# Performance work log

Hardware: AMD Instinct MI355X
Metric: run time of the kernel (lower is better)

Reference implementation:

```python
import jax, jax.numpy as jnp
import numpy as np

B, NUM, NVAR = 2048, 100, 11
NUM_OBS, NC = 10, 3
T_FIN = 10.0
RHO_OBS = 1.0; RHO_INEQ = 1.0; RHO_LANE = 1.0; RHO_PROJ = 1.0
W_SMOOTH = 20.0; W_VDES = 2.0; W_YDES = 1.0
A_EGO = 3.0; B_EGO = 1.5; MARGIN = 0.2
V_MIN = 0.001; V_MAX = 18.0; A_MAX = 6.0
MAXITER = 5
H = 256

def _basis():
    s = np.linspace(0.0, 1.0, NUM)
    j = np.arange(NVAR)
    P = s[:, None] ** j[None, :]
    Pd = np.zeros((NUM, NVAR)); Pdd = np.zeros((NUM, NVAR))
    Pd[:, 1:] = j[1:][None, :] * s[:, None] ** (j[1:] - 1)[None, :]
    Pdd[:, 2:] = (j[2:] * (j[2:] - 1))[None, :] * s[:, None] ** (j[2:] - 2)[None, :]
    return (jnp.asarray(P, jnp.float32), jnp.asarray(Pd / T_FIN, jnp.float32),
            jnp.asarray(Pdd / (T_FIN ** 2), jnp.float32))

P, PDOT, PDDOT = _basis()
A_EQ_X = jnp.stack([P[0], PDOT[0], PDDOT[0], P[-1]])   # [4, NVAR]
A_EQ_Y = jnp.stack([P[0], PDOT[0], PDDOT[0]])          # [3, NVAR]
PTP = P.T @ P

def _kkt_inv(Q, A):
    m = A.shape[0]
    K = jnp.concatenate([jnp.concatenate([Q, A.T], axis=1),
                         jnp.concatenate([A, jnp.zeros((m, m), jnp.float32)], axis=1)], axis=0)
    return jnp.linalg.inv(K)

# ADMM cost: rho_proj*I + smoothness + rho_obs*A_obs^T A_obs + rho_ineq*(Pdot^T Pdot + Pddot^T Pddot)
Q_COMMON = (RHO_PROJ + W_SMOOTH) * jnp.eye(NVAR, dtype=jnp.float32) \
    + RHO_OBS * NUM_OBS * NC * PTP \
    + RHO_INEQ * (PDOT.T @ PDOT + PDDOT.T @ PDDOT)
KKT_X = _kkt_inv(Q_COMMON, A_EQ_X)
KKT_Y = _kkt_inv(Q_COMMON + 2.0 * RHO_LANE * PTP, A_EQ_Y)   # A_lane = [P; -P]
# x_init QP (smoothness + v_des / y_des tracking)
Q_IX = W_SMOOTH * jnp.eye(NVAR, dtype=jnp.float32) + W_VDES * (PDOT.T @ PDOT)
KKT_IX = _kkt_inv(Q_IX, A_EQ_X)
KKT_IY = _kkt_inv(Q_IX + W_YDES * PTP, A_EQ_Y)


def _forward(init_state_ego, goal_des, closest_obs, psi_obs, dim_x_obs, dim_y_obs,
             y_ub, y_lb, gru_W_ih, gru_W_hh, gru_b, gru_h0,
             mlp_W1, mlp_b1, mlp_W2, mlp_b2):
    b = init_state_ego.shape[0]
    x0, y0, vx0, vy0, ax0, ay0 = (init_state_ego[:, i] for i in range(6))
    b_eq_x = jnp.stack([x0, vx0, ax0, goal_des[:, 0]], axis=1)   # [B,4]
    b_eq_y = jnp.stack([y0, vy0, ay0], axis=1)                    # [B,3]

    # ---- obstacle circle trajectories (static obstacles, vx=vy=0) ----
    xo = closest_obs[:, :NUM_OBS]; yo = closest_obs[:, NUM_OBS:2 * NUM_OBS]   # [B,O]
    r = jnp.stack([jnp.zeros_like(dim_x_obs),
                   (dim_x_obs - dim_y_obs) / 2,
                   -(dim_x_obs - dim_y_obs) / 2], axis=2)                      # [B,O,3]
    x_circ = xo[:, :, None] + r * jnp.cos(psi_obs)[:, :, None]                # [B,O,3]
    y_circ = yo[:, :, None] + r * jnp.sin(psi_obs)[:, :, None]
    shape4 = (b, NUM_OBS, NC, NUM)
    x_obs_f = jnp.broadcast_to(x_circ[..., None], shape4).reshape(b, -1)      # [B,O*C*T]
    y_obs_f = jnp.broadcast_to(y_circ[..., None], shape4).reshape(b, -1)
    rad = dim_y_obs / 2
    a_obs = jnp.broadcast_to((A_EGO + rad + MARGIN)[:, :, None, None], shape4).reshape(b, -1)
    b_obs = jnp.broadcast_to((B_EGO + rad + MARGIN)[:, :, None, None], shape4).reshape(b, -1)

    # ---- GRU context over obstacles -> learned lambda init ----
    feats = jnp.stack([xo, yo, dim_x_obs, dim_y_obs, psi_obs], axis=2)        # [B,O,5]
    def gru_step(h, x):
        gx = x @ gru_W_ih + gru_b
        gh = h @ gru_W_hh
        z = jax.nn.sigmoid(gx[:, :H] + gh[:, :H])
        rg = jax.nn.sigmoid(gx[:, H:2 * H] + gh[:, H:2 * H])
        n = jnp.tanh(gx[:, 2 * H:] + rg * gh[:, 2 * H:])
        return (1.0 - z) * n + z * h, None
    hT, _ = jax.lax.scan(gru_step, jnp.broadcast_to(gru_h0, (b, H)), jnp.swapaxes(feats, 0, 1))
    lam = jax.nn.relu(hT @ mlp_W1 + mlp_b1) @ mlp_W2 + mlp_b2                 # [B,2*NVAR]
    lam_x, lam_y = lam[:, :NVAR], lam[:, NVAR:]

    # ---- x_init: equality-constrained smoothness/tracking QP ----
    v_des = jnp.sqrt(vx0 ** 2 + vy0 ** 2)
    lin_ix = W_VDES * v_des[:, None] * jnp.sum(PDOT, axis=0)[None, :]
    lin_iy = W_YDES * goal_des[:, 1:2] * jnp.sum(P, axis=0)[None, :]
    c_x0 = (jnp.concatenate([lin_ix, b_eq_x], 1) @ KKT_IX.T)[:, :NVAR]
    c_y0 = (jnp.concatenate([lin_iy, b_eq_y], 1) @ KKT_IY.T)[:, :NVAR]

    b_lane = jnp.concatenate([y_ub[:, None] * jnp.ones((1, NUM), jnp.float32),
                              -y_lb[:, None] * jnp.ones((1, NUM), jnp.float32)], axis=1)  # [B,2T]

    def AobsT(v):   # A_obs^T v, v: [B, O*C*T] -> [B, NVAR]
        return v.reshape(b, NUM_OBS * NC, NUM).sum(axis=1) @ P

    def step(carry, _):
        c_x, c_y, lx, ly = carry
        x = c_x @ P.T; xd = c_x @ PDOT.T; xdd = c_x @ PDDOT.T
        y = c_y @ P.T; yd = c_y @ PDOT.T; ydd = c_y @ PDDOT.T
        wc = jnp.tile(x, (1, NUM_OBS * NC)) - x_obs_f
        ws = jnp.tile(y, (1, NUM_OBS * NC)) - y_obs_f
        alpha_o = jnp.arctan2(ws * a_obs, wc * b_obs)
        ca, sa = jnp.cos(alpha_o), jnp.sin(alpha_o)
        c1 = RHO_OBS * (a_obs ** 2 * ca ** 2 + b_obs ** 2 * sa ** 2)
        c2 = RHO_OBS * (a_obs * wc * ca + b_obs * ws * sa)
        d_o = jnp.maximum(1.0, c2 / c1)
        alpha_v = jnp.clip(jnp.arctan2(yd, xd), -0.41, 0.41)
        cv, sv = jnp.cos(alpha_v), jnp.sin(alpha_v)
        d_v = jnp.clip(xd * cv + yd * sv, V_MIN, V_MAX)
        alpha_a = jnp.arctan2(ydd + 1e-4, xdd + 1e-4)
        caa, saa = jnp.cos(alpha_a), jnp.sin(alpha_a)
        d_a = jnp.clip(xdd * caa + ydd * saa, 0.0, A_MAX)
        # targets
        b_ox = x_obs_f + a_obs * d_o * ca; b_oy = y_obs_f + b_obs * d_o * sa
        b_vx = d_v * cv; b_vy = d_v * sv
        b_ax = d_a * caa; b_ay = d_a * saa
        b_lane_aug = jnp.minimum(jnp.concatenate([y, -y], 1), b_lane)  # slack-augmented
        top_x = lx + RHO_PROJ * c_x0 + RHO_OBS * AobsT(b_ox) + RHO_INEQ * (b_vx @ PDOT + b_ax @ PDDOT)
        top_y = ly + RHO_PROJ * c_y0 + RHO_OBS * AobsT(b_oy) + RHO_INEQ * (b_vy @ PDOT + b_ay @ PDDOT) \
            + RHO_LANE * ((b_lane_aug[:, :NUM] - b_lane_aug[:, NUM:]) @ P)
        c_xn = (jnp.concatenate([top_x, b_eq_x], 1) @ KKT_X.T)[:, :NVAR]
        c_yn = (jnp.concatenate([top_y, b_eq_y], 1) @ KKT_Y.T)[:, :NVAR]
        # residuals / Lagrange multiplier updates
        xn = c_xn @ P.T; yn = c_yn @ P.T
        res_ox = jnp.tile(xn, (1, NUM_OBS * NC)) - b_ox
        res_oy = jnp.tile(yn, (1, NUM_OBS * NC)) - b_oy
        lxn = lx - RHO_OBS * AobsT(res_ox) \
            - RHO_INEQ * ((c_xn @ PDOT.T - b_vx) @ PDOT + (c_xn @ PDDOT.T - b_ax) @ PDDOT)
        res_lane = jnp.concatenate([yn, -yn], 1) - b_lane_aug
        lyn = ly - RHO_OBS * AobsT(res_oy) \
            - RHO_INEQ * ((c_yn @ PDOT.T - b_vy) @ PDOT + (c_yn @ PDDOT.T - b_ay) @ PDDOT) \
            - RHO_LANE * ((res_lane[:, :NUM] - res_lane[:, NUM:]) @ P)
        return (c_xn, c_yn, lxn, lyn), None

    (c_x, c_y, lam_x, lam_y), _ = jax.lax.scan(step, (c_x0, c_y0, lam_x, lam_y),
                                               None, length=MAXITER)
    return jnp.concatenate([c_x, c_y], axis=1)   # [B, 2*NVAR]


def setup_inputs() -> dict:
    key = jax.random.key(0)
    ks = jax.random.split(key, 12)
    d = {
        'init_state_ego': jax.random.normal(ks[0], (B, 6), jnp.float32),
        'goal_des': jax.random.normal(ks[1], (B, 2), jnp.float32),
        'closest_obs': jax.random.normal(ks[2], (B, 2 * NUM_OBS), jnp.float32),
        'psi_obs': jax.random.normal(ks[3], (B, NUM_OBS), jnp.float32),
        'dim_x_obs': jax.random.uniform(ks[4], (B, NUM_OBS), jnp.float32),
        'dim_y_obs': jax.random.uniform(ks[5], (B, NUM_OBS), jnp.float32),
        'y_ub': jnp.ones((B,), jnp.float32),
        'y_lb': jnp.zeros((B,), jnp.float32),
        'gru_W_ih': jax.random.normal(ks[6], (5, 3 * H), jnp.float32) / np.sqrt(5.0),
        'gru_W_hh': jax.random.normal(ks[7], (H, 3 * H), jnp.float32) / np.sqrt(float(H)),
        'gru_b': jnp.zeros((3 * H,), jnp.float32),
        'gru_h0': jax.random.normal(ks[8], (H,), jnp.float32) * 0.1,
        'mlp_W1': jax.random.normal(ks[9], (H, 512), jnp.float32) / np.sqrt(float(H)),
        'mlp_b1': jnp.zeros((512,), jnp.float32),
        'mlp_W2': jax.random.normal(ks[10], (512, 2 * NVAR), jnp.float32) / np.sqrt(512.0),
        'mlp_b2': jnp.zeros((2 * NVAR,), jnp.float32),
    }
    return d


def reference(init_state_ego, goal_des, closest_obs, psi_obs, dim_x_obs, dim_y_obs,
              y_ub, y_lb, gru_W_ih, gru_W_hh, gru_b, gru_h0,
              mlp_W1, mlp_b1, mlp_W2, mlp_b2):
    return _forward(init_state_ego, goal_des, closest_obs, psi_obs, dim_x_obs, dim_y_obs,
                    y_ub, y_lb, gru_W_ih, gru_W_hh, gru_b, gru_h0,
                    mlp_W1, mlp_b1, mlp_W2, mlp_b2)
```

## Files before the change

### kernel.cpp

```cpp
#include <hip/hip_runtime.h>
#include <math.h>

typedef short bf16x8 __attribute__((ext_vector_type(8)));
typedef float f32x4 __attribute__((ext_vector_type(4)));

__device__ __forceinline__ unsigned short f2bf(float x) {
  union { float f; unsigned u; } v; v.f = x;
  unsigned r = v.u + 0x7FFFu + ((v.u >> 16) & 1u);
  return (unsigned short)(r >> 16);
}
__device__ __forceinline__ float bf2f(unsigned short h) {
  union { unsigned u; float f; } v; v.u = ((unsigned)h) << 16; return v.f;
}

#define WS_WHHT 0u
#define WS_W1T  393216u
#define WS_HA   655360u
#define WS_HB   2752512u
#define WS_ACTS 4849664u
#define WS_LAM  6946816u
#define WS_KKT  7127040u
#define WS_SUMS 7129856u

__global__ __launch_bounds__(256) void convert_weights(
    const float* __restrict__ Whh, const float* __restrict__ W1,
    unsigned short* __restrict__ WhhT, unsigned short* __restrict__ W1T)
{
  int idx = blockIdx.x * 256 + threadIdx.x;
  if (idx < 768 * 256) {
    int n = idx >> 8, k = idx & 255;
    WhhT[idx] = f2bf(Whh[k * 768 + n]);
  } else {
    int j = idx - 768 * 256;
    int n = j >> 8, k = j & 255;
    W1T[j] = f2bf(W1[k * 512 + n]);
  }
}

__global__ __launch_bounds__(256) void setup_kkt(float* __restrict__ kkt_out,
                                                 float* __restrict__ sums_out)
{
  __shared__ double S[21];
  __shared__ double aug[15][32];
  __shared__ double fbuf[15];
  const int mat = blockIdx.x;
  const int n = (mat == 0 || mat == 2) ? 15 : 14;
  const int twoN = 2 * n;
  if (threadIdx.x == 0) {
    for (int m = 0; m < 21; ++m) S[m] = 0.0;
    for (int s = 0; s < 100; ++s) {
      double t = s * (1.0 / 99.0);
      double p = 1.0;
      for (int m = 0; m < 21; ++m) { S[m] += p; p *= t; }
    }
  }
  __syncthreads();
  for (int idx = threadIdx.x; idx < n * twoN; idx += 256) {
    int r = idx / twoN, c = idx % twoN;
    double v;
    if (c >= n) v = (c - n == r) ? 1.0 : 0.0;
    else if (r < 11 && c < 11) {
      double ptp = S[r + c];
      double pdp = (r >= 1 && c >= 1) ? ((double)(r * c) / 100.0) * S[r + c - 2] : 0.0;
      double pddp = (r >= 2 && c >= 2) ? ((double)(r*(r-1)) * (double)(c*(c-1)) / 10000.0) * S[r + c - 4] : 0.0;
      double dg = (r == c) ? 1.0 : 0.0;
      if (mat == 0)      v = 21.0*dg + 30.0*ptp + pdp + pddp;
      else if (mat == 1) v = 21.0*dg + 32.0*ptp + pdp + pddp;
      else if (mat == 2) v = 20.0*dg + 2.0*pdp;
      else               v = 20.0*dg + 2.0*pdp + ptp;
    } else if (r >= 11 && c >= 11) v = 0.0;
    else {
      int ar = (r >= 11) ? (r - 11) : (c - 11);
      int ac = (r >= 11) ? c : r;
      v = (ar == 0) ? ((ac == 0) ? 1.0 : 0.0)
        : (ar == 1) ? ((ac == 1) ? 0.1 : 0.0)
        : (ar == 2) ? ((ac == 2) ? 0.02 : 0.0)
        : 1.0;
    }
    aug[r][c] = v;
  }
  __syncthreads();
  for (int p = 0; p < n; ++p) {
    double pv = aug[p][p];
    __syncthreads();
    double inv = 1.0 / pv;
    for (int c = threadIdx.x; c < twoN; c += 256) aug[p][c] *= inv;
    __syncthreads();
    if (threadIdx.x < n) fbuf[threadIdx.x] = aug[threadIdx.x][p];
    __syncthreads();
    for (int idx = threadIdx.x; idx < n * twoN; idx += 256) {
      int r = idx / twoN, c = idx % twoN;
      if (r != p) aug[r][c] -= fbuf[r] * aug[p][c];
    }
    __syncthreads();
  }
  for (int idx = threadIdx.x; idx < 11 * n; idx += 256) {
    int r = idx / n, c = idx % n;
    kkt_out[mat * 176 + r * 16 + c] = (float)aug[r][n + c];
  }
  if (mat == 0 && threadIdx.x < 11) {
    int j = threadIdx.x;
    sums_out[j] = (float)S[j];
    sums_out[11 + j] = (j >= 1) ? (float)((double)j / 10.0 * S[j - 1]) : 0.f;
  }
}

__global__ __launch_bounds__(256) void gru_step(
    const float* __restrict__ Hin, float* __restrict__ Hout,
    const unsigned short* __restrict__ WhhT,
    const float* __restrict__ Wih, const float* __restrict__ gbias,
    const float* __restrict__ h0,
    const float* __restrict__ obs, const float* __restrict__ dimx,
    const float* __restrict__ dimy, const float* __restrict__ psi,
    int step)
{
  __shared__ __align__(16) unsigned short Alds[8192];
  const int tid = threadIdx.x;
  const int m0 = blockIdx.x * 32;
  const int c0 = blockIdx.y * 64;
  const bool s0 = (step == 0);

  for (int i = 0; i < 4; ++i) {
    int c = tid + 256 * i;
    int kc = c >> 7, rem = c & 127;
    int row = rem >> 2, g = rem & 3;
    int k = kc * 32 + g * 8;
    const float* src = s0 ? (h0 + k) : (Hin + (size_t)(m0 + row) * 256 + k);
    float4 f0 = *(const float4*)(src);
    float4 f1 = *(const float4*)(src + 4);
    union { unsigned short u[8]; int4 v; } pk;
    pk.u[0] = f2bf(f0.x); pk.u[1] = f2bf(f0.y); pk.u[2] = f2bf(f0.z); pk.u[3] = f2bf(f0.w);
    pk.u[4] = f2bf(f1.x); pk.u[5] = f2bf(f1.y); pk.u[6] = f2bf(f1.z); pk.u[7] = f2bf(f1.w);
    *(int4*)(&Alds[c * 8]) = pk.v;
  }
  __syncthreads();

  const int lane = tid & 63, w = tid >> 6;
  const int l15 = lane & 15, g4 = lane >> 4;
  const int ncol = c0 + w * 16 + l15;

  f32x4 zero4 = {0.f, 0.f, 0.f, 0.f};
  f32x4 acc[2][3];
  for (int a = 0; a < 2; ++a)
    for (int g = 0; g < 3; ++g) acc[a][g] = zero4;

  for (int kc = 0; kc < 8; ++kc) {
    bf16x8 a0 = *(const bf16x8*)(&Alds[(kc * 128 + l15 * 4 + g4) * 8]);
    bf16x8 a1 = *(const bf16x8*)(&Alds[(kc * 128 + (16 + l15) * 4 + g4) * 8]);
    int kk = kc * 32 + g4 * 8;
    #pragma unroll
    for (int gate = 0; gate < 3; ++gate) {
      bf16x8 bfrag = *(const bf16x8*)(&WhhT[(size_t)(gate * 256 + ncol) * 256 + kk]);
      acc[0][gate] = __builtin_amdgcn_mfma_f32_16x16x32_bf16(a0, bfrag, acc[0][gate], 0, 0, 0);
      acc[1][gate] = __builtin_amdgcn_mfma_f32_16x16x32_bf16(a1, bfrag, acc[1][gate], 0, 0, 0);
    }
  }

  float wz[5], wr[5], wn[5];
  #pragma unroll
  for (int f = 0; f < 5; ++f) {
    wz[f] = Wih[f * 768 + ncol];
    wr[f] = Wih[f * 768 + 256 + ncol];
    wn[f] = Wih[f * 768 + 512 + ncol];
  }
  float bz = gbias[ncol], br = gbias[256 + ncol], bn = gbias[512 + ncol];

  #pragma unroll
  for (int mi = 0; mi < 2; ++mi) {
    #pragma unroll
    for (int reg = 0; reg < 4; ++reg) {
      int row = m0 + mi * 16 + g4 * 4 + reg;
      float t0 = obs[row * 20 + step];
      float t1 = obs[row * 20 + 10 + step];
      float t2 = dimx[row * 10 + step];
      float t3 = dimy[row * 10 + step];
      float t4 = psi[row * 10 + step];
      float gz = bz + t0*wz[0] + t1*wz[1] + t2*wz[2] + t3*wz[3] + t4*wz[4];
      float gr = br + t0*wr[0] + t1*wr[1] + t2*wr[2] + t3*wr[3] + t4*wr[4];
      float gn = bn + t0*wn[0] + t1*wn[1] + t2*wn[2] + t3*wn[3] + t4*wn[4];
      float z = 1.f / (1.f + __expf(-(gz + acc[mi][0][reg])));
      float r = 1.f / (1.f + __expf(-(gr + acc[mi][1][reg])));
      float nn = tanhf(gn + r * acc[mi][2][reg]);
      float hold = s0 ? h0[ncol] : Hin[(size_t)row * 256 + ncol];
      Hout[(size_t)row * 256 + ncol] = (1.f - z) * nn + z * hold;
    }
  }
}

__global__ __launch_bounds__(256) void mlp1(
    const float* __restrict__ Hin, const unsigned short* __restrict__ W1T,
    const float* __restrict__ b1, unsigned short* __restrict__ acts)
{
  __shared__ __align__(16) unsigned short Alds[8192];
  const int tid = threadIdx.x;
  const int m0 = blockIdx.x * 32;
  const int c0 = blockIdx.y * 128;

  for (int i = 0; i < 4; ++i) {
    int c = tid + 256 * i;
    int kc = c >> 7, rem = c & 127;
    int row = rem >> 2, g = rem & 3;
    int k = kc * 32 + g * 8;
    const float* src = Hin + (size_t)(m0 + row) * 256 + k;
    float4 f0 = *(const float4*)(src);
    float4 f1 = *(const float4*)(src + 4);
    union { unsigned short u[8]; int4 v; } pk;
    pk.u[0] = f2bf(f0.x); pk.u[1] = f2bf(f0.y); pk.u[2] = f2bf(f0.z); pk.u[3] = f2bf(f0.w);
    pk.u[4] = f2bf(f1.x); pk.u[5] = f2bf(f1.y); pk.u[6] = f2bf(f1.z); pk.u[7] = f2bf(f1.w);
    *(int4*)(&Alds[c * 8]) = pk.v;
  }
  __syncthreads();

  const int lane = tid & 63, w = tid >> 6;
  const int l15 = lane & 15, g4 = lane >> 4;
  const int nbase = c0 + w * 32 + l15;

  f32x4 zero4 = {0.f, 0.f, 0.f, 0.f};
  f32x4 acc[2][2];
  for (int a = 0; a < 2; ++a)
    for (int g = 0; g < 2; ++g) acc[a][g] = zero4;

  for (int kc = 0; kc < 8; ++kc) {
    bf16x8 a0 = *(const bf16x8*)(&Alds[(kc * 128 + l15 * 4 + g4) * 8]);
    bf16x8 a1 = *(const bf16x8*)(&Alds[(kc * 128 + (16 + l15) * 4 + g4) * 8]);
    int kk = kc * 32 + g4 * 8;
    #pragma unroll
    for (int cf = 0; cf < 2; ++cf) {
      bf16x8 bfrag = *(const bf16x8*)(&W1T[(size_t)(nbase + cf * 16) * 256 + kk]);
      acc[0][cf] = __builtin_amdgcn_mfma_f32_16x16x32_bf16(a0, bfrag, acc[0][cf], 0, 0, 0);
      acc[1][cf] = __builtin_amdgcn_mfma_f32_16x16x32_bf16(a1, bfrag, acc[1][cf], 0, 0, 0);
    }
  }

  #pragma unroll
  for (int mi = 0; mi < 2; ++mi) {
    #pragma unroll
    for (int cf = 0; cf < 2; ++cf) {
      int col = nbase + cf * 16;
      float bb = b1[col];
      #pragma unroll
      for (int reg = 0; reg < 4; ++reg) {
        int row = m0 + mi * 16 + g4 * 4 + reg;
        float v = acc[mi][cf][reg] + bb;
        acts[(size_t)row * 512 + col] = f2bf(fmaxf(v, 0.f));
      }
    }
  }
}

__global__ __launch_bounds__(256) void mlp2(
    const unsigned short* __restrict__ acts, const float* __restrict__ W2,
    const float* __restrict__ b2, float* __restrict__ lam)
{
  __shared__ unsigned short Ablk[8 * 520];
  __shared__ float W2s[512 * 22];
  const int tid = threadIdx.x;
  const int m0 = blockIdx.x * 8;
  for (int i = tid; i < 4096; i += 256) {
    int r = i >> 9, k = i & 511;
    Ablk[r * 520 + k] = acts[(size_t)(m0 + r) * 512 + k];
  }
  for (int i = tid; i < 11264; i += 256) W2s[i] = W2[i];
  __syncthreads();
  if (tid < 176) {
    int row = tid / 22, col = tid - (tid / 22) * 22;
    float s = b2[col];
    const unsigned short* ap = &Ablk[row * 520];
    for (int k = 0; k < 512; ++k) s += bf2f(ap[k]) * W2s[k * 22 + col];
    lam[(size_t)(m0 + row) * 22 + col] = s;
  }
}

__global__ __launch_bounds__(128) void solver(
    const float* __restrict__ ise, const float* __restrict__ goal,
    const float* __restrict__ obs, const float* __restrict__ psi,
    const float* __restrict__ dimx, const float* __restrict__ dimy,
    const float* __restrict__ yub, const float* __restrict__ ylb,
    const float* __restrict__ lam, const float* __restrict__ kkt,
    const float* __restrict__ sums, float* __restrict__ out)
{
  __shared__ float Pt[3][11][104];
  __shared__ float red[7][104];
  __shared__ float redout[7][11];
  __shared__ float cx[11], cy[11], lx[11], ly[11], cx0[11], cy0[11];
  __shared__ float cxn[11], cyn[11];
  __shared__ float rhsx[15], rhsy[14];
  __shared__ float xc[30], yc[30], ao[10], bo[10], ao2[10], bo2[10];

  const int b = blockIdx.x;
  const int tid = threadIdx.x;

  if (tid < 100) {
    float t = tid * (1.0f / 99.0f);
    float tjm2 = 0.f, tjm1 = 0.f, tj = 1.f;
    #pragma unroll
    for (int j = 0; j < 11; ++j) {
      Pt[0][j][tid] = tj;
      Pt[1][j][tid] = 0.1f * (float)j * tjm1;
      Pt[2][j][tid] = 0.01f * (float)(j * (j - 1)) * tjm2;
      tjm2 = tjm1; tjm1 = tj; tj *= t;
    }
  }
  if (tid < 10) {
    int o = tid;
    float xo = obs[b * 20 + o], yo = obs[b * 20 + 10 + o];
    float dx = dimx[b * 10 + o], dy = dimy[b * 10 + o], ps = psi[b * 10 + o];
    float sp, cp;
    __sincosf(ps, &sp, &cp);
    float r1 = 0.5f * (dx - dy);
    xc[o * 3] = xo; xc[o * 3 + 1] = xo + r1 * cp; xc[o * 3 + 2] = xo - r1 * cp;
    yc[o * 3] = yo; yc[o * 3 + 1] = yo + r1 * sp; yc[o * 3 + 2] = yo - r1 * sp;
    float rad = 0.5f * dy;
    float av = 3.2f + rad, bv = 1.7f + rad;
    ao[o] = av; bo[o] = bv; ao2[o] = av * av; bo2[o] = bv * bv;
  }
  if (tid < 11) { lx[tid] = lam[b * 22 + tid]; ly[tid] = lam[b * 22 + 11 + tid]; }
  const float vx0 = ise[b * 6 + 2], vy0 = ise[b * 6 + 3];
  if (tid == 0) {
    float x0 = ise[b * 6 + 0], y0 = ise[b * 6 + 1];
    float ax0 = ise[b * 6 + 4], ay0 = ise[b * 6 + 5];
    rhsx[11] = x0; rhsx[12] = vx0; rhsx[13] = ax0; rhsx[14] = goal[b * 2 + 0];
    rhsy[11] = y0; rhsy[12] = vy0; rhsy[13] = ay0;
  }
  {
    float vdes = sqrtf(vx0 * vx0 + vy0 * vy0);
    float gy = goal[b * 2 + 1];
    if (tid < 11) { rhsx[tid] = 2.f * vdes * sums[11 + tid]; rhsy[tid] = gy * sums[tid]; }
  }
  const float yU = yub[b], yL = ylb[b];
  __syncthreads();
  if (tid < 11) {
    const float* K = kkt + 2 * 176 + tid * 16;
    float s = 0.f;
    #pragma unroll
    for (int j = 0; j < 15; ++j) s += K[j] * rhsx[j];
    cx0[tid] = s; cx[tid] = s;
  } else if (tid >= 16 && tid < 27) {
    int i = tid - 16;
    const float* K = kkt + 3 * 176 + i * 16;
    float s = 0.f;
    #pragma unroll
    for (int j = 0; j < 14; ++j) s += K[j] * rhsy[j];
    cy0[i] = s; cy[i] = s;
  }
  __syncthreads();

  float Sbx = 0.f, Sby = 0.f, bvx = 0.f, bvy = 0.f, bax = 0.f, bay = 0.f, lane_t = 0.f;
  for (int it = 0; it < 5; ++it) {
    if (tid < 100) {
      float t = tid * (1.0f / 99.0f);
      float x = 0, y = 0, xd = 0, yd = 0, xdd = 0, ydd = 0;
      {
        float tjm2 = 0, tjm1 = 0, tj = 1;
        #pragma unroll
        for (int j = 0; j < 11; ++j) {
          float cj = cx[j], dj = cy[j];
          x += cj * tj; y += dj * tj;
          float pd = 0.1f * (float)j * tjm1;
          xd += cj * pd; yd += dj * pd;
          float pdd = 0.01f * (float)(j * (j - 1)) * tjm2;
          xdd += cj * pdd; ydd += dj * pdd;
          tjm2 = tjm1; tjm1 = tj; tj *= t;
        }
      }
      Sbx = 0.f; Sby = 0.f;
      for (int oi = 0; oi < 10; ++oi) {
        float A = ao[oi], B = bo[oi], A2 = ao2[oi], B2 = bo2[oi];
        #pragma unroll
        for (int cc = 0; cc < 3; ++cc) {
          int o = oi * 3 + cc;
          float xcc = xc[o], ycc = yc[o];
          float wc = x - xcc, wsv = y - ycc;
          float p = wsv * A, q = wc * B;
          float rin = rsqrtf(p * p + q * q + 1e-20f);
          float ca = q * rin, sa = p * rin;
          float c1 = A2 * ca * ca + B2 * sa * sa;
      float c2 = A * wc * ca + B * wsv * sa;
          float d = fmaxf(1.f, __fdividef(c2, c1));
          Sbx += xcc + A * d * ca;
          Sby += ycc + B * d * sa;
        }
      }
      float av = atan2f(yd, xd);
      float cv, sv;
      if (fabsf(av) > 0.41f) { cv = 0.91712081f; sv = copysignf(0.39860934f, av); }
      else { float ri = rsqrtf(fmaxf(xd * xd + yd * yd, 1e-24f)); cv = xd * ri; sv = yd * ri; }
      float dv = fminf(fmaxf(xd * cv + yd * sv, 0.001f), 18.f);
      bvx = dv * cv; bvy = dv * sv;
      float qa = xdd + 1e-4f, pa = ydd + 1e-4f;
      float ria = rsqrtf(pa * pa + qa * qa + 1e-30f);
      float caa = qa * ria, saa = pa * ria;
      float da = fminf(fmaxf(xdd * caa + ydd * saa, 0.f), 6.f);
      bax = da * caa; bay = da * saa;
      lane_t = fminf(y, yU) - fminf(-y, -yL);
      red[0][tid] = Sbx; red[1][tid] = Sby; red[2][tid] = bvx; red[3][tid] = bvy;
      red[4][tid] = bax; red[5][tid] = bay; red[6][tid] = lane_t;
    }
    __syncthreads();
    if (tid < 77) {
      int a = tid / 11, j = tid - a * 11;
      int wt = (a < 2) ? 0 : (a < 4) ? 1 : (a < 6) ? 2 : 0;
      const float4* rp = (const float4*)(&red[a][0]);
      const float4* wp = (const float4*)(&Pt[wt][j][0]);
      float s = 0.f;
      for (int k = 0; k < 25; ++k) {
        float4 rv = rp[k], wv = wp[k];
        s += rv.x * wv.x + rv.y * wv.y + rv.z * wv.z + rv.w * wv.w;
      }
      redout[a][j] = s;
    }
    __syncthreads();
    if (tid < 11) rhsx[tid] = lx[tid] + cx0[tid] + redout[0][tid] + redout[2][tid] + redout[4][tid];
    else if (tid >= 16 && tid < 27) {
      int j = tid - 16;
      rhsy[j] = ly[j] + cy0[j] + redout[1][j] + redout[3][j] + redout[5][j] + redout[6][j];
    }
    __syncthreads();
    if (tid < 11) {
      const float* K = kkt + tid * 16;
      float s = 0.f;
      #pragma unroll
      for (int j = 0; j < 15; ++j) s += K[j] * rhsx[j];
      cxn[tid] = s;
    } else if (tid >= 16 && tid < 27) {
      int i = tid - 16;
      const float* K = kkt + 176 + i * 16;
      float s = 0.f;
      #pragma unroll
      for (int j = 0; j < 14; ++j) s += K[j] * rhsy[j];
      cyn[i] = s;
    }
    __syncthreads();
    if (tid < 100) {
      float t = tid * (1.0f / 99.0f);
      float xn = 0, yn = 0, xdn = 0, ydn = 0, xddn = 0, yddn = 0;
      {
        float tjm2 = 0, tjm1 = 0, tj = 1;
        #pragma unroll
        for (int j = 0; j < 11; ++j) {
          float cj = cxn[j], dj = cyn[j];
          xn += cj * tj; yn += dj * tj;
          float pd = 0.1f * (float)j * tjm1;
          xdn += cj * pd; ydn += dj * pd;
          float pdd = 0.01f * (float)(j * (j - 1)) * tjm2;
          xddn += cj * pdd; yddn += dj * pdd;
          tjm2 = tjm1; tjm1 = tj; tj *= t;
        }
      }
      red[0][tid] = 30.f * xn - Sbx;
      red[1][tid] = xdn - bvx;
      red[2][tid] = xddn - bax;
      red[3][tid] = 30.f * yn - Sby;
      red[4][tid] = ydn - bvy;
      red[5][tid] = yddn - bay;
      red[6][tid] = 2.f * yn - lane_t;
    }
    __syncthreads();
    if (tid < 77) {
      int a = tid / 11, j = tid - a * 11;
      int wt = (a == 0 || a == 3 || a == 6) ? 0 : (a == 1 || a == 4) ? 1 : 2;
      const float4* rp = (const float4*)(&red[a][0]);
      const float4* wp = (const float4*)(&Pt[wt][j][0]);
      float s = 0.f;
      for (int k = 0; k < 25; ++k) {
        float4 rv = rp[k], wv = wp[k];
        s += rv.x * wv.x + rv.y * wv.y + rv.z * wv.z + rv.w * wv.w;
      }
      redout[a][j] = s;
    }
    __syncthreads();
    if (tid < 11) { lx[tid] -= redout[0][tid] + redout[1][tid] + redout[2][tid]; cx[tid] = cxn[tid]; }
    else if (tid >= 16 && tid < 27) {
      int j = tid - 16;
      ly[j] -= redout[3][j] + redout[4][j] + redout[5][j] + redout[6][j];
      cy[j] = cyn[j];
    }
    __syncthreads();
  }
  if (tid < 11) out[b * 22 + tid] = cx[tid];
  else if (tid >= 16 && tid < 27) out[b * 22 + 11 + (tid - 16)] = cy[tid - 16];
}

extern "C" void kernel_launch(void* const* d_in, const int* in_sizes, int n_in,
                              void* d_out, int out_size, void* d_ws, size_t ws_size,
                              hipStream_t stream) {
  const float* ise  = (const float*)d_in[0];
  const float* goal = (const float*)d_in[1];
  const float* obs  = (const float*)d_in[2];
  const float* psi  = (const float*)d_in[3];
  const float* dimx = (const float*)d_in[4];
  const float* dimy = (const float*)d_in[5];
  const float* yub  = (const float*)d_in[6];
  const float* ylb  = (const float*)d_in[7];
  const float* Wih  = (const float*)d_in[8];
  const float* Whh  = (const float*)d_in[9];
  const float* gb   = (const float*)d_in[10];
  const float* h0   = (const float*)d_in[11];
  const float* W1   = (const float*)d_in[12];
  const float* b1   = (const float*)d_in[13];
  const float* W2   = (const float*)d_in[14];
  const float* b2   = (const float*)d_in[15];

  char* ws = (char*)d_ws;
  unsigned short* WhhT = (unsigned short*)(ws + WS_WHHT);
  unsigned short* W1T  = (unsigned short*)(ws + WS_W1T);
  float* HA   = (float*)(ws + WS_HA);
  float* HB   = (float*)(ws + WS_HB);
  unsigned short* acts = (unsigned short*)(ws + WS_ACTS);
  float* lamb = (float*)(ws + WS_LAM);
  float* kkt  = (float*)(ws + WS_KKT);
  float* sums = (float*)(ws + WS_SUMS);

  convert_weights<<<1280, 256, 0, stream>>>(Whh, W1, WhhT, W1T);
  setup_kkt<<<4, 256, 0, stream>>>(kkt, sums);
  for (int s = 0; s < 10; ++s) {
    const float* hin = (s % 2 == 0) ? HB : HA;
    float* hout = (s % 2 == 0) ? HA : HB;
    gru_step<<<dim3(64, 4), 256, 0, stream>>>(hin, hout, WhhT, Wih, gb, h0,
                                              obs, dimx, dimy, psi, s);
  }
  mlp1<<<dim3(64, 4), 256, 0, stream>>>(HB, W1T, b1, acts);
  mlp2<<<256, 256, 0, stream>>>(acts, W2, b2, lamb);
  solver<<<2048, 128, 0, stream>>>(ise, goal, obs, psi, dimx, dimy, yub, ylb,
                                   lamb, kkt, sums, (float*)d_out);
  (void)in_sizes; (void)n_in; (void)out_size; (void)ws_size;
}
```

Baseline: 286.8 us.

## Fuse GRU steps and MLP into one persistent kernel and simplify solver projections

Replaces ten per-step GRU launches plus two MLP kernels with a single kernel where each block keeps its 32-row hidden state in LDS/registers across all steps. The input projection and bias are folded into an augmented bf16 weight matrix so they go through MFMA, and the second MLP layer moves from a scalar loop to MFMA. Weight prep and KKT setup merge into one launch. The solver's obstacle projection is rewritten algebraically without a divide, and the velocity clip drops atan2 for a slope comparison. The cost is only 64 blocks for the recurrent part, so the GPU is heavily underoccupied, and the new algebraic forms may round slightly differently.

```diff
diff --git a/kernel.cpp b/kernel.cpp
--- a/kernel.cpp
+++ b/kernel.cpp
@@ -9,265 +9,267 @@
   unsigned r = v.u + 0x7FFFu + ((v.u >> 16) & 1u);
   return (unsigned short)(r >> 16);
 }
-__device__ __forceinline__ float bf2f(unsigned short h) {
-  union { unsigned u; float f; } v; v.u = ((unsigned)h) << 16; return v.f;
-}
-
-#define WS_WHHT 0u
-#define WS_W1T  393216u
-#define WS_HA   655360u
-#define WS_HB   2752512u
-#define WS_ACTS 4849664u
-#define WS_LAM  6946816u
-#define WS_KKT  7127040u
-#define WS_SUMS 7129856u
-
-__global__ __launch_bounds__(256) void convert_weights(
-    const float* __restrict__ Whh, const float* __restrict__ W1,
-    unsigned short* __restrict__ WhhT, unsigned short* __restrict__ W1T)
-{
-  int idx = blockIdx.x * 256 + threadIdx.x;
-  if (idx < 768 * 256) {
-    int n = idx >> 8, k = idx & 255;
-    WhhT[idx] = f2bf(Whh[k * 768 + n]);
-  } else {
-    int j = idx - 768 * 256;
-    int n = j >> 8, k = j & 255;
-    W1T[j] = f2bf(W1[k * 512 + n]);
-  }
-}
-
-__global__ __launch_bounds__(256) void setup_kkt(float* __restrict__ kkt_out,
-                                                 float* __restrict__ sums_out)
+
+#define WS_WAUG 0u
+#define WS_W1T  442368u
+#define WS_W2T  704512u
+#define WS_LAM  737280u
+#define WS_KKT  917504u
+#define WS_SUMS 920320u
+
+__global__ __launch_bounds__(256) void prep(
+    const float* __restrict__ Whh, const float* __restrict__ Wih,
+    const float* __restrict__ gb, const float* __restrict__ W1,
+    const float* __restrict__ W2,
+    unsigned short* __restrict__ Waug, unsigned short* __restrict__ W1T,
+    unsigned short* __restrict__ W2T,
+    float* __restrict__ kkt_out, float* __restrict__ sums_out)
 {
   __shared__ double S[21];
   __shared__ double aug[15][32];
   __shared__ double fbuf[15];
-  const int mat = blockIdx.x;
-  const int n = (mat == 0 || mat == 2) ? 15 : 14;
-  const int twoN = 2 * n;
-  if (threadIdx.x == 0) {
-    for (int m = 0; m < 21; ++m) S[m] = 0.0;
-    for (int s = 0; s < 100; ++s) {
-      double t = s * (1.0 / 99.0);
-      double p = 1.0;
-      for (int m = 0; m < 21; ++m) { S[m] += p; p *= t; }
-    }
-  }
-  __syncthreads();
-  for (int idx = threadIdx.x; idx < n * twoN; idx += 256) {
-    int r = idx / twoN, c = idx % twoN;
-    double v;
-    if (c >= n) v = (c - n == r) ? 1.0 : 0.0;
-    else if (r < 11 && c < 11) {
-      double ptp = S[r + c];
-      double pdp = (r >= 1 && c >= 1) ? ((double)(r * c) / 100.0) * S[r + c - 2] : 0.0;
-      double pddp = (r >= 2 && c >= 2) ? ((double)(r*(r-1)) * (double)(c*(c-1)) / 10000.0) * S[r + c - 4] : 0.0;
-      double dg = (r == c) ? 1.0 : 0.0;
-      if (mat == 0)      v = 21.0*dg + 30.0*ptp + pdp + pddp;
-      else if (mat == 1) v = 21.0*dg + 32.0*ptp + pdp + pddp;
-      else if (mat == 2) v = 20.0*dg + 2.0*pdp;
-      else               v = 20.0*dg + 2.0*pdp + ptp;
-    } else if (r >= 11 && c >= 11) v = 0.0;
-    else {
-      int ar = (r >= 11) ? (r - 11) : (c - 11);
-      int ac = (r >= 11) ? c : r;
-      v = (ar == 0) ? ((ac == 0) ? 1.0 : 0.0)
-        : (ar == 1) ? ((ac == 1) ? 0.1 : 0.0)
-        : (ar == 2) ? ((ac == 2) ? 0.02 : 0.0)
-        : 1.0;
-    }
-    aug[r][c] = v;
-  }
-  __syncthreads();
-  for (int p = 0; p < n; ++p) {
-    double pv = aug[p][p];
-    __syncthreads();
-    double inv = 1.0 / pv;
-    for (int c = threadIdx.x; c < twoN; c += 256) aug[p][c] *= inv;
-    __syncthreads();
-    if (threadIdx.x < n) fbuf[threadIdx.x] = aug[threadIdx.x][p];
+  if (blockIdx.x < 4) {
+    const int mat = blockIdx.x;
+    const int n = (mat == 0 || mat == 2) ? 15 : 14;
+    const int twoN = 2 * n;
+    if (threadIdx.x == 0) {
+      for (int m = 0; m < 21; ++m) S[m] = 0.0;
+      for (int s = 0; s < 100; ++s) {
+        double t = s * (1.0 / 99.0);
+        double p = 1.0;
+        for (int m = 0; m < 21; ++m) { S[m] += p; p *= t; }
+      }
+    }
     __syncthreads();
     for (int idx = threadIdx.x; idx < n * twoN; idx += 256) {
       int r = idx / twoN, c = idx % twoN;
-      if (r != p) aug[r][c] -= fbuf[r] * aug[p][c];
-    }
-    __syncthreads();
-  }
-  for (int idx = threadIdx.x; idx < 11 * n; idx += 256) {
-    int r = idx / n, c = idx % n;
-    kkt_out[mat * 176 + r * 16 + c] = (float)aug[r][n + c];
-  }
-  if (mat == 0 && threadIdx.x < 11) {
-    int j = threadIdx.x;
-    sums_out[j] = (float)S[j];
-    sums_out[11 + j] = (j >= 1) ? (float)((double)j / 10.0 * S[j - 1]) : 0.f;
+      double v;
+      if (c >= n) v = (c - n == r) ? 1.0 : 0.0;
+      else if (r < 11 && c < 11) {
+        double ptp = S[r + c];
+        double pdp = (r >= 1 && c >= 1) ? ((double)(r * c) / 100.0) * S[r + c - 2] : 0.0;
+        double pddp = (r >= 2 && c >= 2) ? ((double)(r*(r-1)) * (double)(c*(c-1)) / 10000.0) * S[r + c - 4] : 0.0;
+        double dg = (r == c) ? 1.0 : 0.0;
+        if (mat == 0)      v = 21.0*dg + 30.0*ptp + pdp + pddp;
+        else if (mat == 1) v = 21.0*dg + 32.0*ptp + pdp + pddp;
+        else if (mat == 2) v = 20.0*dg + 2.0*pdp;
+        else               v = 20.0*dg + 2.0*pdp + ptp;
+      } else if (r >= 11 && c >= 11) v = 0.0;
+      else {
+        int ar = (r >= 11) ? (r - 11) : (c - 11);
+        int ac = (r >= 11) ? c : r;
+        v = (ar == 0) ? ((ac == 0) ? 1.0 : 0.0)
+          : (ar == 1) ? ((ac == 1) ? 0.1 : 0.0)
+          : (ar == 2) ? ((ac == 2) ? 0.02 : 0.0)
+          : 1.0;
+      }
+      aug[r][c] = v;
+    }
+    __syncthreads();
+    for (int p = 0; p < n; ++p) {
+      double pv = aug[p][p];
+      __syncthreads();
+      double inv = 1.0 / pv;
+      for (int c = threadIdx.x; c < twoN; c += 256) aug[p][c] *= inv;
+      __syncthreads();
+      if (threadIdx.x < n) fbuf[threadIdx.x] = aug[threadIdx.x][p];
+      __syncthreads();
+      for (int idx = threadIdx.x; idx < n * twoN; idx += 256) {
+        int r = idx / twoN, c = idx % twoN;
+        if (r != p) aug[r][c] -= fbuf[r] * aug[p][c];
+      }
+      __syncthreads();
+    }
+    for (int idx = threadIdx.x; idx < 11 * n; idx += 256) {
+      int r = idx / n, c = idx % n;
+      kkt_out[mat * 176 + r * 16 + c] = (float)aug[r][n + c];
+    }
+    if (mat == 0 && threadIdx.x < 11) {
+      int j = threadIdx.x;
+      sums_out[j] = (float)S[j];
+      sums_out[11 + j] = (j >= 1) ? (float)((double)j / 10.0 * S[j - 1]) : 0.f;
+    }
+    return;
+  }
+  int idx = (blockIdx.x - 4) * 256 + threadIdx.x;
+  if (idx < 221184) {
+    int col = idx / 288, k = idx - col * 288;
+    float v;
+    if (k < 256)       v = Whh[k * 768 + col];
+    else if (k < 261)  v = Wih[(k - 256) * 768 + col];
+    else if (k == 261) v = gb[col];
+    else               v = 0.f;
+    Waug[idx] = f2bf(v);
+  } else if (idx < 221184 + 131072) {
+    int j = idx - 221184;
+    int col = j >> 8, k = j & 255;
+    W1T[j] = f2bf(W1[k * 512 + col]);
+  } else if (idx < 221184 + 131072 + 16384) {
+    int j = idx - 352256;
+    int col = j >> 9, k = j & 511;
+    W2T[j] = f2bf(col < 22 ? W2[k * 22 + col] : 0.f);
   }
 }
 
-__global__ __launch_bounds__(256) void gru_step(
-    const float* __restrict__ Hin, float* __restrict__ Hout,
-    const unsigned short* __restrict__ WhhT,
-    const float* __restrict__ Wih, const float* __restrict__ gbias,
-    const float* __restrict__ h0,
+#define MFMA __builtin_amdgcn_mfma_f32_16x16x32_bf16
+__global__ __launch_bounds__(512, 1) void gru_mlp(
+    const float* __restrict__ h0, const unsigned short* __restrict__ Waug,
     const float* __restrict__ obs, const float* __restrict__ dimx,
     const float* __restrict__ dimy, const float* __restrict__ psi,
-    int step)
+    const unsigned short* __restrict__ W1T, const float* __restrict__ b1,
+    const unsigned short* __restrict__ W2T, const float* __restrict__ b2,
+    float* __restrict__ lam)
 {
-  __shared__ __align__(16) unsigned short Alds[8192];
+  __shared__ __align__(16) unsigned short A[9216];
+  __shared__ __align__(16) unsigned short acts[16384];
+  __shared__ float fl[32][52];
   const int tid = threadIdx.x;
   const int m0 = blockIdx.x * 32;
-  const int c0 = blockIdx.y * 64;
-  const bool s0 = (step == 0);
-
-  for (int i = 0; i < 4; ++i) {
-    int c = tid + 256 * i;
-    int kc = c >> 7, rem = c & 127;
-    int row = rem >> 2, g = rem & 3;
-    int k = kc * 32 + g * 8;
-    const float* src = s0 ? (h0 + k) : (Hin + (size_t)(m0 + row) * 256 + k);
-    float4 f0 = *(const float4*)(src);
-    float4 f1 = *(const float4*)(src + 4);
-    union { unsigned short u[8]; int4 v; } pk;
-    pk.u[0] = f2bf(f0.x); pk.u[1] = f2bf(f0.y); pk.u[2] = f2bf(f0.z); pk.u[3] = f2bf(f0.w);
-    pk.u[4] = f2bf(f1.x); pk.u[5] = f2bf(f1.y); pk.u[6] = f2bf(f1.z); pk.u[7] = f2bf(f1.w);
-    *(int4*)(&Alds[c * 8]) = pk.v;
-  }
-  __syncthreads();
-
   const int lane = tid & 63, w = tid >> 6;
   const int l15 = lane & 15, g4 = lane >> 4;
-  const int ncol = c0 + w * 16 + l15;
-
-  f32x4 zero4 = {0.f, 0.f, 0.f, 0.f};
-  f32x4 acc[2][3];
-  for (int a = 0; a < 2; ++a)
-    for (int g = 0; g < 3; ++g) acc[a][g] = zero4;
-
-  for (int kc = 0; kc < 8; ++kc) {
-    bf16x8 a0 = *(const bf16x8*)(&Alds[(kc * 128 + l15 * 4 + g4) * 8]);
-    bf16x8 a1 = *(const bf16x8*)(&Alds[(kc * 128 + (16 + l15) * 4 + g4) * 8]);
-    int kk = kc * 32 + g4 * 8;
-    #pragma unroll
-    for (int gate = 0; gate < 3; ++gate) {
-      bf16x8 bfrag = *(const bf16x8*)(&WhhT[(size_t)(gate * 256 + ncol) * 256 + kk]);
-      acc[0][gate] = __builtin_amdgcn_mfma_f32_16x16x32_bf16(a0, bfrag, acc[0][gate], 0, 0, 0);
-      acc[1][gate] = __builtin_amdgcn_mfma_f32_16x16x32_bf16(a1, bfrag, acc[1][gate], 0, 0, 0);
-    }
-  }
-
-  float wz[5], wr[5], wn[5];
+
+  for (int i = tid; i < 1600; i += 512) {
+    int row = i / 50, r = i - row * 50;
+    int f = r / 10, s = r - f * 10;
+    int gr = m0 + row;
+    float v = (f == 0) ? obs[gr * 20 + s] : (f == 1) ? obs[gr * 20 + 10 + s]
+            : (f == 2) ? dimx[gr * 10 + s] : (f == 3) ? dimy[gr * 10 + s]
+            : psi[gr * 10 + s];
+    fl[row][f * 10 + s] = v;
+  }
+  for (int i = tid; i < 8192; i += 512) {
+    int col = ((i >> 10) << 5) + (i & 31);
+    A[i] = f2bf(h0[col]);
+  }
+  for (int i = tid; i < 1024; i += 512) A[8192 + i] = 0;
+  if (tid < 192) {
+    int row = tid / 6, e = tid - row * 6;
+    float v = (e < 5) ? fl[row][e * 10 + 0] : 1.0f;
+    A[(8 * 32 + row) * 32 + e] = f2bf(v);
+  }
+  float hreg[2][2][4];
   #pragma unroll
-  for (int f = 0; f < 5; ++f) {
-    wz[f] = Wih[f * 768 + ncol];
-    wr[f] = Wih[f * 768 + 256 + ncol];
-    wn[f] = Wih[f * 768 + 512 + ncol];
-  }
-  float bz = gbias[ncol], br = gbias[256 + ncol], bn = gbias[512 + ncol];
-
-  #pragma unroll
-  for (int mi = 0; mi < 2; ++mi) {
-    #pragma unroll
-    for (int reg = 0; reg < 4; ++reg) {
-      int row = m0 + mi * 16 + g4 * 4 + reg;
-      float t0 = obs[row * 20 + step];
-      float t1 = obs[row * 20 + 10 + step];
-      float t2 = dimx[row * 10 + step];
-      float t3 = dimy[row * 10 + step];
-      float t4 = psi[row * 10 + step];
-      float gz = bz + t0*wz[0] + t1*wz[1] + t2*wz[2] + t3*wz[3] + t4*wz[4];
-      float gr = br + t0*wr[0] + t1*wr[1] + t2*wr[2] + t3*wr[3] + t4*wr[4];
-      float gn = bn + t0*wn[0] + t1*wn[1] + t2*wn[2] + t3*wn[3] + t4*wn[4];
-      float z = 1.f / (1.f + __expf(-(gz + acc[mi][0][reg])));
-      float r = 1.f / (1.f + __expf(-(gr + acc[mi][1][reg])));
-      float nn = tanhf(gn + r * acc[mi][2][reg]);
-      float hold = s0 ? h0[ncol] : Hin[(size_t)row * 256 + ncol];
-      Hout[(size_t)row * 256 + ncol] = (1.f - z) * nn + z * hold;
-    }
-  }
-}
-
-__global__ __launch_bounds__(256) void mlp1(
-    const float* __restrict__ Hin, const unsigned short* __restrict__ W1T,
-    const float* __restrict__ b1, unsigned short* __restrict__ acts)
-{
-  __shared__ __align__(16) unsigned short Alds[8192];
-  const int tid = threadIdx.x;
-  const int m0 = blockIdx.x * 32;
-  const int c0 = blockIdx.y * 128;
-
-  for (int i = 0; i < 4; ++i) {
-    int c = tid + 256 * i;
-    int kc = c >> 7, rem = c & 127;
-    int row = rem >> 2, g = rem & 3;
-    int k = kc * 32 + g * 8;
-    const float* src = Hin + (size_t)(m0 + row) * 256 + k;
-    float4 f0 = *(const float4*)(src);
-    float4 f1 = *(const float4*)(src + 4);
-    union { unsigned short u[8]; int4 v; } pk;
-    pk.u[0] = f2bf(f0.x); pk.u[1] = f2bf(f0.y); pk.u[2] = f2bf(f0.z); pk.u[3] = f2bf(f0.w);
-    pk.u[4] = f2bf(f1.x); pk.u[5] = f2bf(f1.y); pk.u[6] = f2bf(f1.z); pk.u[7] = f2bf(f1.w);
-    *(int4*)(&Alds[c * 8]) = pk.v;
+  for (int nt = 0; nt < 2; ++nt) {
+    float hv = h0[w * 32 + nt * 16 + l15];
+    #pragma unroll
+    for (int mi = 0; mi < 2; ++mi)
+      #pragma unroll
+      for (int rg = 0; rg < 4; ++rg) hreg[mi][nt][rg] = hv;
   }
   __syncthreads();
 
-  const int lane = tid & 63, w = tid >> 6;
-  const int l15 = lane & 15, g4 = lane >> 4;
-  const int nbase = c0 + w * 32 + l15;
-
-  f32x4 zero4 = {0.f, 0.f, 0.f, 0.f};
-  f32x4 acc[2][2];
-  for (int a = 0; a < 2; ++a)
-    for (int g = 0; g < 2; ++g) acc[a][g] = zero4;
-
-  for (int kc = 0; kc < 8; ++kc) {
-    bf16x8 a0 = *(const bf16x8*)(&Alds[(kc * 128 + l15 * 4 + g4) * 8]);
-    bf16x8 a1 = *(const bf16x8*)(&Alds[(kc * 128 + (16 + l15) * 4 + g4) * 8]);
-    int kk = kc * 32 + g4 * 8;
-    #pragma unroll
-    for (int cf = 0; cf < 2; ++cf) {
-      bf16x8 bfrag = *(const bf16x8*)(&W1T[(size_t)(nbase + cf * 16) * 256 + kk]);
-      acc[0][cf] = __builtin_amdgcn_mfma_f32_16x16x32_bf16(a0, bfrag, acc[0][cf], 0, 0, 0);
-      acc[1][cf] = __builtin_amdgcn_mfma_f32_16x16x32_bf16(a1, bfrag, acc[1][cf], 0, 0, 0);
-    }
-  }
-
-  #pragma unroll
-  for (int mi = 0; mi < 2; ++mi) {
-    #pragma unroll
-    for (int cf = 0; cf < 2; ++cf) {
-      int col = nbase + cf * 16;
-      float bb = b1[col];
-      #pragma unroll
-      for (int reg = 0; reg < 4; ++reg) {
-        int row = m0 + mi * 16 + g4 * 4 + reg;
-        float v = acc[mi][cf][reg] + bb;
-        acts[(size_t)row * 512 + col] = f2bf(fmaxf(v, 0.f));
-      }
-    }
-  }
-}
-
-__global__ __launch_bounds__(256) void mlp2(
-    const unsigned short* __restrict__ acts, const float* __restrict__ W2,
-    const float* __restrict__ b2, float* __restrict__ lam)
-{
-  __shared__ unsigned short Ablk[8 * 520];
-  __shared__ float W2s[512 * 22];
-  const int tid = threadIdx.x;
-  const int m0 = blockIdx.x * 8;
-  for (int i = tid; i < 4096; i += 256) {
-    int r = i >> 9, k = i & 511;
-    Ablk[r * 520 + k] = acts[(size_t)(m0 + r) * 512 + k];
-  }
-  for (int i = tid; i < 11264; i += 256) W2s[i] = W2[i];
+  for (int s = 0; s < 10; ++s) {
+    f32x4 az[2][2], ar_[2][2], anh[2][2], anx[2][2];
+    #pragma unroll
+    for (int mi = 0; mi < 2; ++mi)
+      #pragma unroll
+      for (int nt = 0; nt < 2; ++nt) {
+        az[mi][nt] = (f32x4){0.f,0.f,0.f,0.f}; ar_[mi][nt] = (f32x4){0.f,0.f,0.f,0.f};
+        anh[mi][nt] = (f32x4){0.f,0.f,0.f,0.f}; anx[mi][nt] = (f32x4){0.f,0.f,0.f,0.f};
+      }
+    #pragma unroll
+    for (int kc = 0; kc < 9; ++kc) {
+      bf16x8 a0 = *(const bf16x8*)&A[((kc * 32 + l15) * 4 + g4) * 8];
+      bf16x8 a1 = *(const bf16x8*)&A[((kc * 32 + 16 + l15) * 4 + g4) * 8];
+      int kk = kc * 32 + g4 * 8;
+      #pragma unroll
+      for (int nt = 0; nt < 2; ++nt) {
+        int col = w * 32 + nt * 16 + l15;
+        bf16x8 bz = *(const bf16x8*)&Waug[(size_t)col * 288 + kk];
+        bf16x8 br = *(const bf16x8*)&Waug[(size_t)(256 + col) * 288 + kk];
+        bf16x8 bn = *(const bf16x8*)&Waug[(size_t)(512 + col) * 288 + kk];
+        az[0][nt] = MFMA(a0, bz, az[0][nt], 0, 0, 0);
+        az[1][nt] = MFMA(a1, bz, az[1][nt], 0, 0, 0);
+        ar_[0][nt] = MFMA(a0, br, ar_[0][nt], 0, 0, 0);
+        ar_[1][nt] = MFMA(a1, br, ar_[1][nt], 0, 0, 0);
+        if (kc < 8) {
+          anh[0][nt] = MFMA(a0, bn, anh[0][nt], 0, 0, 0);
+          anh[1][nt] = MFMA(a1, bn, anh[1][nt], 0, 0, 0);
+        } else {
+          anx[0][nt] = MFMA(a0, bn, anx[0][nt], 0, 0, 0);
+          anx[1][nt] = MFMA(a1, bn, anx[1][nt], 0, 0, 0);
+        }
+      }
+    }
+    __syncthreads();
+    #pragma unroll
+    for (int mi = 0; mi < 2; ++mi)
+      #pragma unroll
+      for (int nt = 0; nt < 2; ++nt) {
+        int col = w * 32 + nt * 16 + l15;
+        #pragma unroll
+        for (int rg = 0; rg < 4; ++rg) {
+          int row = mi * 16 + g4 * 4 + rg;
+          float z = __builtin_amdgcn_rcpf(1.f + __expf(-az[mi][nt][rg]));
+          float r = __builtin_amdgcn_rcpf(1.f + __expf(-ar_[mi][nt][rg]));
+          float narg = anx[mi][nt][rg] + r * anh[mi][nt][rg];
+          float nn = 1.f - 2.f * __builtin_amdgcn_rcpf(__expf(2.f * narg) + 1.f);
+          float hnew = (1.f - z) * nn + z * hreg[mi][nt][rg];
+          hreg[mi][nt][rg] = hnew;
+          A[((w * 32 + row) * 4 + ((col >> 3) & 3)) * 8 + (col & 7)] = f2bf(hnew);
+        }
+      }
+    if (s < 9 && tid < 192) {
+      int row = tid / 6, e = tid - row * 6;
+      float v = (e < 5) ? fl[row][e * 10 + s + 1] : 1.0f;
+      A[(8 * 32 + row) * 32 + e] = f2bf(v);
+    }
+    __syncthreads();
+  }
+
+  {
+    f32x4 acc1[2][4];
+    #pragma unroll
+    for (int mi = 0; mi < 2; ++mi)
+      #pragma unroll
+      for (int nt = 0; nt < 4; ++nt) acc1[mi][nt] = (f32x4){0.f,0.f,0.f,0.f};
+    #pragma unroll
+    for (int kc = 0; kc < 8; ++kc) {
+      bf16x8 a0 = *(const bf16x8*)&A[((kc * 32 + l15) * 4 + g4) * 8];
+      bf16x8 a1 = *(const bf16x8*)&A[((kc * 32 + 16 + l15) * 4 + g4) * 8];
+      int kk = kc * 32 + g4 * 8;
+      #pragma unroll
+      for (int nt = 0; nt < 4; ++nt) {
+        int col = w * 64 + nt * 16 + l15;
+        bf16x8 b = *(const bf16x8*)&W1T[(size_t)col * 256 + kk];
+        acc1[0][nt] = MFMA(a0, b, acc1[0][nt], 0, 0, 0);
+        acc1[1][nt] = MFMA(a1, b, acc1[1][nt], 0, 0, 0);
+      }
+    }
+    #pragma unroll
+    for (int mi = 0; mi < 2; ++mi)
+      #pragma unroll
+      for (int nt = 0; nt < 4; ++nt) {
+        int col = w * 64 + nt * 16 + l15;
+        float bb = b1[col];
+        #pragma unroll
+        for (int rg = 0; rg < 4; ++rg) {
+          int row = mi * 16 + g4 * 4 + rg;
+          float v = fmaxf(acc1[mi][nt][rg] + bb, 0.f);
+          acts[(((col >> 5) * 32 + row) * 4 + ((col >> 3) & 3)) * 8 + (col & 7)] = f2bf(v);
+        }
+      }
+  }
   __syncthreads();
-  if (tid < 176) {
-    int row = tid / 22, col = tid - (tid / 22) * 22;
-    float s = b2[col];
-    const unsigned short* ap = &Ablk[row * 520];
-    for (int k = 0; k < 512; ++k) s += bf2f(ap[k]) * W2s[k * 22 + col];
-    lam[(size_t)(m0 + row) * 22 + col] = s;
+
+  if (w < 4) {
+    int mi = w >> 1, nt = w & 1;
+    int col = nt * 16 + l15;
+    f32x4 a2 = {0.f, 0.f, 0.f, 0.f};
+    #pragma unroll
+    for (int kc = 0; kc < 16; ++kc) {
+      bf16x8 a = *(const bf16x8*)&acts[((kc * 32 + mi * 16 + l15) * 4 + g4) * 8];
+      bf16x8 b = *(const bf16x8*)&W2T[(size_t)col * 512 + kc * 32 + g4 * 8];
+      a2 = MFMA(a, b, a2, 0, 0, 0);
+    }
+    if (col < 22) {
+      float bb = b2[col];
+      #pragma unroll
+      for (int rg = 0; rg < 4; ++rg) {
+        int row = m0 + mi * 16 + g4 * 4 + rg;
+        lam[row * 22 + col] = a2[rg] + bb;
+      }
+    }
   }
 }
 
@@ -279,13 +281,13 @@
     const float* __restrict__ lam, const float* __restrict__ kkt,
     const float* __restrict__ sums, float* __restrict__ out)
 {
-  __shared__ float Pt[3][11][104];
-  __shared__ float red[7][104];
+  __shared__ __align__(16) float Pt[3][11][108];
+  __shared__ __align__(16) float red[7][108];
   __shared__ float redout[7][11];
   __shared__ float cx[11], cy[11], lx[11], ly[11], cx0[11], cy0[11];
   __shared__ float cxn[11], cyn[11];
   __shared__ float rhsx[15], rhsy[14];
-  __shared__ float xc[30], yc[30], ao[10], bo[10], ao2[10], bo2[10];
+  __shared__ float xc[30], yc[30], sa_[10], sb_[10], sab[10], sab2[10];
 
   const int b = blockIdx.x;
   const int tid = threadIdx.x;
@@ -312,7 +314,7 @@
     yc[o * 3] = yo; yc[o * 3 + 1] = yo + r1 * sp; yc[o * 3 + 2] = yo - r1 * sp;
     float rad = 0.5f * dy;
     float av = 3.2f + rad, bv = 1.7f + rad;
-    ao[o] = av; bo[o] = bv; ao2[o] = av * av; bo2[o] = bv * bv;
+    sa_[o] = av; sb_[o] = bv; sab[o] = av * bv; sab2[o] = av * bv * av * bv;
   }
   if (tid < 11) { lx[tid] = lam[b * 22 + tid]; ly[tid] = lam[b * 22 + 11 + tid]; }
   const float vx0 = ise[b * 6 + 2], vy0 = ise[b * 6 + 3];
@@ -365,25 +367,24 @@
       }
       Sbx = 0.f; Sby = 0.f;
       for (int oi = 0; oi < 10; ++oi) {
-        float A = ao[oi], B = bo[oi], A2 = ao2[oi], B2 = bo2[oi];
+        float A = sa_[oi], B = sb_[oi], AB = sab[oi], AB2 = sab2[oi];
         #pragma unroll
         for (int cc = 0; cc < 3; ++cc) {
           int o = oi * 3 + cc;
           float xcc = xc[o], ycc = yc[o];
           float wc = x - xcc, wsv = y - ycc;
           float p = wsv * A, q = wc * B;
-          float rin = rsqrtf(p * p + q * q + 1e-20f);
-          float ca = q * rin, sa = p * rin;
-          float c1 = A2 * ca * ca + B2 * sa * sa;
-      float c2 = A * wc * ca + B * wsv * sa;
-          float d = fmaxf(1.f, __fdividef(c2, c1));
-          Sbx += xcc + A * d * ca;
-          Sby += ycc + B * d * sa;
+          float h2 = p * p + q * q;
+          float rin = rsqrtf(h2 + 1e-20f);
+          float sc = AB * rin;
+          bool outside = h2 >= AB2;
+          Sbx += outside ? x : fmaf(wc, sc, xcc);
+          Sby += outside ? y : fmaf(wsv, sc, ycc);
         }
       }
-      float av = atan2f(yd, xd);
+      bool clipv = (xd <= 0.f) || (fabsf(yd) > xd * 0.43463135f);
       float cv, sv;
-      if (fabsf(av) > 0.41f) { cv = 0.91712081f; sv = copysignf(0.39860934f, av); }
+      if (clipv) { cv = 0.91712081f; sv = copysignf(0.39860934f, yd); }
       else { float ri = rsqrtf(fmaxf(xd * xd + yd * yd, 1e-24f)); cv = xd * ri; sv = yd * ri; }
       float dv = fminf(fmaxf(xd * cv + yd * sv, 0.001f), 18.f);
       bvx = dv * cv; bvy = dv * sv;
@@ -502,25 +503,15 @@
   const float* b2   = (const float*)d_in[15];
 
   char* ws = (char*)d_ws;
-  unsigned short* WhhT = (unsigned short*)(ws + WS_WHHT);
+  unsigned short* Waug = (unsigned short*)(ws + WS_WAUG);
   unsigned short* W1T  = (unsigned short*)(ws + WS_W1T);
-  float* HA   = (float*)(ws + WS_HA);
-  float* HB   = (float*)(ws + WS_HB);
-  unsigned short* acts = (unsigned short*)(ws + WS_ACTS);
+  unsigned short* W2T  = (unsigned short*)(ws + WS_W2T);
   float* lamb = (float*)(ws + WS_LAM);
   float* kkt  = (float*)(ws + WS_KKT);
   float* sums = (float*)(ws + WS_SUMS);
 
-  convert_weights<<<1280, 256, 0, stream>>>(Whh, W1, WhhT, W1T);
-  setup_kkt<<<4, 256, 0, stream>>>(kkt, sums);
-  for (int s = 0; s < 10; ++s) {
-    const float* hin = (s % 2 == 0) ? HB : HA;
-    float* hout = (s % 2 == 0) ? HA : HB;
-    gru_step<<<dim3(64, 4), 256, 0, stream>>>(hin, hout, WhhT, Wih, gb, h0,
-                                              obs, dimx, dimy, psi, s);
-  }
-  mlp1<<<dim3(64, 4), 256, 0, stream>>>(HB, W1T, b1, acts);
-  mlp2<<<256, 256, 0, stream>>>(acts, W2, b2, lamb);
+  prep<<<1444, 256, 0, stream>>>(Whh, Wih, gb, W1, W2, Waug, W1T, W2T, kkt, sums);
+  gru_mlp<<<64, 512, 0, stream>>>(h0, Waug, obs, dimx, dimy, psi, W1T, b1, W2T, b2, lamb);
   solver<<<2048, 128, 0, stream>>>(ise, goal, obs, psi, dimx, dimy, yub, ylb,
                                    lamb, kkt, sums, (float*)d_out);
   (void)in_sizes; (void)n_in; (void)out_size; (void)ws_size;
```

Measured after the change: 265.5 us. 1.08x faster.
